# Kernel tuning notes

Measured on AMD Instinct MI355X. Metric: run time of the kernel, lower is better.

Reference implementation:

```python
import jax, jax.numpy as jnp
import numpy as np

N_NODES = 50000
N_EDGES = 800000
IN_FEATS = 1024
LAYERS = [128, 128]
EPS = 1e-5  # BatchNorm1d eps


def setup_inputs() -> dict:
    key = jax.random.key(0)
    ks = jax.random.split(key, 24)
    inp = {}
    inp["in_feat"] = jax.random.normal(ks[0], (N_NODES, IN_FEATS), jnp.float32)
    inp["src"] = jax.random.randint(ks[1], (N_EDGES,), 0, N_NODES, dtype=jnp.int32)
    inp["dst"] = jax.random.randint(ks[2], (N_EDGES,), 0, N_NODES, dtype=jnp.int32)
    dims = [IN_FEATS] + LAYERS
    i = 3
    for l in range(len(LAYERS)):
        din, dout = dims[l], dims[l + 1]
        s = 1.0 / np.sqrt(din)
        inp[f"W{l}"] = jax.random.uniform(ks[i], (din, dout), jnp.float32, -s, s); i += 1
        inp[f"b{l}"] = jnp.zeros((dout,), jnp.float32)
        inp[f"Wr{l}"] = jax.random.uniform(ks[i], (din, dout), jnp.float32, -s, s); i += 1
        inp[f"br{l}"] = jnp.zeros((dout,), jnp.float32)
        inp[f"gamma{l}"] = jnp.ones((dout,), jnp.float32)
        inp[f"beta{l}"] = jnp.zeros((dout,), jnp.float32)
        inp[f"mean{l}"] = jnp.zeros((dout,), jnp.float32)
        inp[f"var{l}"] = jnp.ones((dout,), jnp.float32)
    s = 1.0 / np.sqrt(LAYERS[-1])
    inp["Wd"] = jax.random.uniform(ks[i], (LAYERS[-1], 2), jnp.float32, -s, s)
    inp["bd"] = jnp.zeros((2,), jnp.float32)
    return inp


def gcn_layer(h, src, dst, W, b, Wr, br, gamma, beta, mean, var):
    # dgllife GCNLayer: GraphConv(norm='none', activation=relu) -> residual -> dropout(id, eval) -> BN(eval)
    msg = (h @ W)[src]                                        # [E, dout] gather of transformed src feats
    agg = jax.ops.segment_sum(msg, dst, num_segments=N_NODES)  # scatter-add to dst nodes
    new = jax.nn.relu(agg + b)                                 # GraphConv bias + activation
    res = jax.nn.relu(h @ Wr + br)                             # residual Linear + activation
    new = new + res
    return (new - mean) * jax.lax.rsqrt(var + EPS) * gamma + beta  # BatchNorm1d eval


def reference(in_feat, src, dst,
              W0, b0, Wr0, br0, gamma0, beta0, mean0, var0,
              W1, b1, Wr1, br1, gamma1, beta1, mean1, var1,
              Wd, bd):
    h = gcn_layer(in_feat, src, dst, W0, b0, Wr0, br0, gamma0, beta0, mean0, var0)
    h = gcn_layer(h, src, dst, W1, b1, Wr1, br1, gamma1, beta1, mean1, var1)
    logits = h @ Wd + bd                                       # [N, 2]
    return jax.nn.softmax(logits, axis=1)
```

## Files before the change

kernel.cpp:

```cpp
#include <hip/hip_runtime.h>
#include <math.h>

#define NNODES 50000
#define NEDGES 800000
#define KIN 1024
#define DH 128

typedef __bf16 bf16x8 __attribute__((ext_vector_type(8)));
typedef float floatx4 __attribute__((ext_vector_type(4)));

__global__ void k_zero2(int* __restrict__ a, int* __restrict__ b, int n) {
  int i = blockIdx.x * blockDim.x + threadIdx.x;
  if (i < n) { a[i] = 0; b[i] = 0; }
}

__global__ void k_hist(const int* __restrict__ dst, int* __restrict__ cnt, int E) {
  int i = blockIdx.x * blockDim.x + threadIdx.x;
  if (i < E) atomicAdd(&cnt[dst[i]], 1);
}

__global__ __launch_bounds__(1024) void k_scan_local(const int* __restrict__ cnt,
                                                     int* __restrict__ row_ptr,
                                                     int* __restrict__ bsum, int n) {
  __shared__ int sd[1024];
  int t = threadIdx.x;
  int i = blockIdx.x * 1024 + t;
  int v = (i < n) ? cnt[i] : 0;
  sd[t] = v;
  __syncthreads();
  for (int off = 1; off < 1024; off <<= 1) {
    int tv = (t >= off) ? sd[t - off] : 0;
    __syncthreads();
    sd[t] += tv;
    __syncthreads();
  }
  if (i < n) row_ptr[i] = sd[t] - v;
  if (t == 1023) bsum[blockIdx.x] = sd[t];
}

__global__ void k_scan_sums(const int* __restrict__ bsum, int* __restrict__ boff,
                            int nb, int* __restrict__ row_ptr, int n) {
  int lane = threadIdx.x;
  int v = (lane < nb) ? bsum[lane] : 0;
  int incl = v;
  for (int off = 1; off < 64; off <<= 1) {
    int t = __shfl_up(incl, off);
    if (lane >= off) incl += t;
  }
  boff[lane] = incl - v;
  if (lane == 63) row_ptr[n] = incl;
}

__global__ void k_scan_add(int* __restrict__ row_ptr, const int* __restrict__ boff, int n) {
  int i = blockIdx.x * blockDim.x + threadIdx.x;
  if (i < n) row_ptr[i] += boff[i >> 10];
}

__global__ void k_fill(const int* __restrict__ src, const int* __restrict__ dst,
                       const int* __restrict__ row_ptr, int* __restrict__ cursor,
                       int* __restrict__ csr_src, int E) {
  int i = blockIdx.x * blockDim.x + threadIdx.x;
  if (i < E) {
    int d = dst[i];
    int pos = row_ptr[d] + atomicAdd(&cursor[d], 1);
    csr_src[pos] = src[i];
  }
}

__global__ __launch_bounds__(256) void k_prepF(const float* __restrict__ W,
                                               const float* __restrict__ Wr,
                                               __bf16* __restrict__ Bf) {
  const int id = blockIdx.x * 256 + threadIdx.x;
  const int lane = id & 63;
  const int ks = (id >> 6) & 1;
  const int nt = (id >> 7) & 15;
  const int kb = id >> 11;
  const int n = nt * 16 + (lane & 15);
  const int k0 = kb * 64 + ks * 32 + (lane >> 4) * 8;
  bf16x8 h;
#pragma unroll
  for (int j = 0; j < 8; ++j) {
    const int k = k0 + j;
    const float v = (n < DH) ? W[(size_t)k * DH + n] : Wr[(size_t)k * DH + (n - DH)];
    h[j] = (__bf16)v;
  }
  *(bf16x8*)&Bf[(size_t)id * 8] = h;
}

template <typename AT, int K>
__global__ __launch_bounds__(256) void k_gemm3(
    const AT* __restrict__ X, const __bf16* __restrict__ Bf,
    const float* __restrict__ br, __bf16* __restrict__ XW,
    float* __restrict__ RES, int M) {
  constexpr unsigned ABYTES = 32u * K * 2u;
  constexpr unsigned SMEM = (ABYTES > 32768u) ? ABYTES : 32768u;
  __shared__ alignas(16) char smem[SMEM];
  __bf16* As = (__bf16*)smem;
  const int tid = threadIdx.x;
  const int lane = tid & 63;
  const int w = tid >> 6;
  const int l15 = lane & 15;
  const int quad = lane >> 4;
  const int bm0 = blockIdx.x * 32;

  {
    const int row = tid >> 3;
    int grow = bm0 + row;
    if (grow > M - 1) grow = M - 1;
    const AT* ap = X + (size_t)grow * K;
#pragma unroll 4
    for (int j = 0; j < K / 64; ++j) {
      const int c = (tid & 7) + 8 * j;
      bf16x8 h;
      if constexpr (sizeof(AT) == 4) {
        const float4 u = *(const float4*)(ap + c * 8);
        const float4 v = *(const float4*)(ap + c * 8 + 4);
        h[0] = (__bf16)u.x; h[1] = (__bf16)u.y; h[2] = (__bf16)u.z; h[3] = (__bf16)u.w;
        h[4] = (__bf16)v.x; h[5] = (__bf16)v.y; h[6] = (__bf16)v.z; h[7] = (__bf16)v.w;
      } else {
        h = *(const bf16x8*)(ap + c * 8);
      }
      const int cs = (c & ~7) | ((c ^ row) & 7);
      *(bf16x8*)&As[(size_t)row * K + (cs << 3)] = h;
    }
  }
  __syncthreads();

  floatx4 acc[2][4];
#pragma unroll
  for (int i = 0; i < 2; ++i)
#pragma unroll
    for (int j = 0; j < 4; ++j) acc[i][j] = (floatx4)0.f;

#pragma unroll 2
  for (int kb = 0; kb < K / 64; ++kb) {
    bf16x8 bfr[4][2];
#pragma unroll
    for (int nt = 0; nt < 4; ++nt)
#pragma unroll
      for (int ks = 0; ks < 2; ++ks) {
        const int ntg = (w << 2) + nt;
        const size_t idx = ((((size_t)kb * 16 + ntg) * 2 + ks) * 64 + lane) * 8;
        bfr[nt][ks] = *(const bf16x8*)(Bf + idx);
      }
    bf16x8 af[2][2];
#pragma unroll
    for (int mt = 0; mt < 2; ++mt)
#pragma unroll
      for (int ks = 0; ks < 2; ++ks) {
        const int row = mt * 16 + l15;
        const int c = kb * 8 + ks * 4 + quad;
        const int cs = (c & ~7) | ((c ^ row) & 7);
        af[mt][ks] = *(const bf16x8*)&As[(size_t)row * K + (cs << 3)];
      }
#pragma unroll
    for (int ks = 0; ks < 2; ++ks)
#pragma unroll
      for (int mt = 0; mt < 2; ++mt)
#pragma unroll
        for (int nt = 0; nt < 4; ++nt)
          acc[mt][nt] = __builtin_amdgcn_mfma_f32_16x16x32_bf16(af[mt][ks], bfr[nt][ks],
                                                                acc[mt][nt], 0, 0, 0);
  }

  __syncthreads();
  float* Cb = (float*)smem;
#pragma unroll
  for (int mt = 0; mt < 2; ++mt)
#pragma unroll
    for (int nt = 0; nt < 4; ++nt)
#pragma unroll
      for (int r = 0; r < 4; ++r)
        Cb[(mt * 16 + quad * 4 + r) * 256 + ((w << 6) + nt * 16 + l15)] = acc[mt][nt][r];
  __syncthreads();
  const int row = tid >> 3;
  const int seg = tid & 7;
  const int grow = bm0 + row;
  if (grow < M) {
    if (seg < 4) {
      const int c0 = seg * 32;
#pragma unroll
      for (int j = 0; j < 4; ++j) {
        const float4 v0 = *(const float4*)&Cb[row * 256 + c0 + j * 8];
        const float4 v1 = *(const float4*)&Cb[row * 256 + c0 + j * 8 + 4];
        bf16x8 h;
        h[0] = (__bf16)v0.x; h[1] = (__bf16)v0.y; h[2] = (__bf16)v0.z; h[3] = (__bf16)v0.w;
        h[4] = (__bf16)v1.x; h[5] = (__bf16)v1.y; h[6] = (__bf16)v1.z; h[7] = (__bf16)v1.w;
        *(bf16x8*)&XW[(size_t)grow * DH + c0 + j * 8] = h;
      }
    } else {
      const int c0 = (seg - 4) * 32;
#pragma unroll
      for (int j = 0; j < 8; ++j) {
        const float4 v = *(const float4*)&Cb[row * 256 + 128 + c0 + j * 4];
        const float4 bb = *(const float4*)&br[c0 + j * 4];
        *(float4*)&RES[(size_t)grow * DH + c0 + j * 4] =
            make_float4(fmaxf(v.x + bb.x, 0.f), fmaxf(v.y + bb.y, 0.f),
                        fmaxf(v.z + bb.z, 0.f), fmaxf(v.w + bb.w, 0.f));
      }
    }
  }
}

template <int MODE>
__global__ __launch_bounds__(256) void k_agg2(
    const __bf16* __restrict__ XW, const float* __restrict__ RES,
    const int* __restrict__ row_ptr, const int* __restrict__ csr_src,
    const float* __restrict__ b, const float* __restrict__ gamma,
    const float* __restrict__ beta, const float* __restrict__ mean,
    const float* __restrict__ var, const float* __restrict__ Wd,
    const float* __restrict__ bd, void* __restrict__ hout, int M) {
  const int node = (blockIdx.x << 2) + (threadIdx.x >> 6);
  const int lane = threadIdx.x & 63;
  if (node >= M) return;
  const int s = row_ptr[node], e = row_ptr[node + 1];
  const unsigned* xw = (const unsigned*)XW;
  float ax = 0.f, ay = 0.f;
  int i = s;
  for (; i + 3 < e; i += 4) {
    const int s0 = csr_src[i], s1 = csr_src[i + 1], s2 = csr_src[i + 2], s3 = csr_src[i + 3];
    const unsigned u0 = xw[(size_t)s0 * 64 + lane];
    const unsigned u1 = xw[(size_t)s1 * 64 + lane];
    const unsigned u2 = xw[(size_t)s2 * 64 + lane];
    const unsigned u3 = xw[(size_t)s3 * 64 + lane];
    ax += __uint_as_float(u0 << 16) + __uint_as_float(u1 << 16) +
          __uint_as_float(u2 << 16) + __uint_as_float(u3 << 16);
    ay += __uint_as_float(u0 & 0xffff0000u) + __uint_as_float(u1 & 0xffff0000u) +
          __uint_as_float(u2 & 0xffff0000u) + __uint_as_float(u3 & 0xffff0000u);
  }
  for (; i < e; ++i) {
    const unsigned u = xw[(size_t)csr_src[i] * 64 + lane];
    ax += __uint_as_float(u << 16);
    ay += __uint_as_float(u & 0xffff0000u);
  }
  const int f0 = lane << 1;
  const float2 bb = *(const float2*)&b[f0];
  const float2 rr = *(const float2*)&RES[(size_t)node * DH + f0];
  const float2 mm = *(const float2*)&mean[f0];
  const float2 vv = *(const float2*)&var[f0];
  const float2 gg = *(const float2*)&gamma[f0];
  const float2 be = *(const float2*)&beta[f0];
  const float x0 = fmaxf(ax + bb.x, 0.f) + rr.x;
  const float x1 = fmaxf(ay + bb.y, 0.f) + rr.y;
  const float y0 = (x0 - mm.x) * rsqrtf(vv.x + 1e-5f) * gg.x + be.x;
  const float y1 = (x1 - mm.y) * rsqrtf(vv.y + 1e-5f) * gg.y + be.y;
  if (MODE == 0) {
    union { __bf16 h[2]; unsigned u; } pk;
    pk.h[0] = (__bf16)y0;
    pk.h[1] = (__bf16)y1;
    ((unsigned*)hout)[(size_t)node * 64 + lane] = pk.u;
  } else {
    const float4 wv = *(const float4*)&Wd[f0 * 2];
    float l0 = y0 * wv.x + y1 * wv.z;
    float l1 = y0 * wv.y + y1 * wv.w;
#pragma unroll
    for (int off = 32; off > 0; off >>= 1) {
      l0 += __shfl_down(l0, off);
      l1 += __shfl_down(l1, off);
    }
    if (lane == 0) {
      l0 += bd[0];
      l1 += bd[1];
      const float m = fmaxf(l0, l1);
      const float e0 = expf(l0 - m), e1 = expf(l1 - m);
      const float inv = 1.f / (e0 + e1);
      float* out = (float*)hout;
      out[(size_t)node * 2] = e0 * inv;
      out[(size_t)node * 2 + 1] = e1 * inv;
    }
  }
}

extern "C" void kernel_launch(void* const* d_in, const int* in_sizes, int n_in,
                              void* d_out, int out_size, void* d_ws, size_t ws_size,
                              hipStream_t stream) {
  const float* in_feat = (const float*)d_in[0];
  const int* src = (const int*)d_in[1];
  const int* dst = (const int*)d_in[2];
  const float* W0 = (const float*)d_in[3];
  const float* b0 = (const float*)d_in[4];
  const float* Wr0 = (const float*)d_in[5];
  const float* br0 = (const float*)d_in[6];
  const float* gamma0 = (const float*)d_in[7];
  const float* beta0 = (const float*)d_in[8];
  const float* mean0 = (const float*)d_in[9];
  const float* var0 = (const float*)d_in[10];
  const float* W1 = (const float*)d_in[11];
  const float* b1 = (const float*)d_in[12];
  const float* Wr1 = (const float*)d_in[13];
  const float* br1 = (const float*)d_in[14];
  const float* gamma1 = (const float*)d_in[15];
  const float* beta1 = (const float*)d_in[16];
  const float* mean1 = (const float*)d_in[17];
  const float* var1 = (const float*)d_in[18];
  const float* Wd = (const float*)d_in[19];
  const float* bd = (const float*)d_in[20];
  float* out = (float*)d_out;

  char* ws = (char*)d_ws;
  size_t off = 0;
  auto alloc = [&](size_t bytes) {
    void* p = ws + off;
    off += (bytes + 255) & ~(size_t)255;
    return p;
  };
  __bf16* XWb = (__bf16*)alloc(sizeof(__bf16) * (size_t)NNODES * DH);
  __bf16* h1 = (__bf16*)alloc(sizeof(__bf16) * (size_t)NNODES * DH);
  float* RES = (float*)alloc(sizeof(float) * (size_t)NNODES * DH);
  int* cnt = (int*)alloc(sizeof(int) * NNODES);
  int* cursor = (int*)alloc(sizeof(int) * NNODES);
  int* row_ptr = (int*)alloc(sizeof(int) * (NNODES + 1));
  int* csr_src = (int*)alloc(sizeof(int) * NEDGES);
  int* bsum = (int*)alloc(sizeof(int) * 64);
  int* boff = (int*)alloc(sizeof(int) * 64);
  __bf16* Bf0 = (__bf16*)alloc(sizeof(__bf16) * 256 * KIN);
  __bf16* Bf1 = (__bf16*)alloc(sizeof(__bf16) * 256 * DH);

  const int nb = (NNODES + 1023) / 1024;
  k_zero2<<<(NNODES + 255) / 256, 256, 0, stream>>>(cnt, cursor, NNODES);
  k_hist<<<(NEDGES + 255) / 256, 256, 0, stream>>>(dst, cnt, NEDGES);
  k_scan_local<<<nb, 1024, 0, stream>>>(cnt, row_ptr, bsum, NNODES);
  k_scan_sums<<<1, 64, 0, stream>>>(bsum, boff, nb, row_ptr, NNODES);
  k_scan_add<<<(NNODES + 255) / 256, 256, 0, stream>>>(row_ptr, boff, NNODES);
  k_fill<<<(NEDGES + 255) / 256, 256, 0, stream>>>(src, dst, row_ptr, cursor, csr_src, NEDGES);

  k_prepF<<<(KIN / 64) * 16 * 2 * 64 / 256, 256, 0, stream>>>(W0, Wr0, Bf0);
  k_prepF<<<(DH / 64) * 16 * 2 * 64 / 256, 256, 0, stream>>>(W1, Wr1, Bf1);

  const int ggrid = (NNODES + 31) / 32;
  const int agrid = (NNODES + 3) / 4;
  k_gemm3<float, KIN><<<ggrid, 256, 0, stream>>>(in_feat, Bf0, br0, XWb, RES, NNODES);
  k_agg2<0><<<agrid, 256, 0, stream>>>(XWb, RES, row_ptr, csr_src, b0, gamma0, beta0,
                                       mean0, var0, nullptr, nullptr, h1, NNODES);
  k_gemm3<__bf16, DH><<<ggrid, 256, 0, stream>>>(h1, Bf1, br1, XWb, RES, NNODES);
  k_agg2<1><<<agrid, 256, 0, stream>>>(XWb, RES, row_ptr, csr_src, b1, gamma1, beta1,
                                       mean1, var1, Wd, bd, out, NNODES);
}
```

Baseline: 567.8 us.

## Load GEMM A fragments directly from global, interleave bf16 residual, shuffle-broadcast edge indices

Result: slower. 625.1 us (+10.1%).

```diff
diff --git a/kernel.cpp b/kernel.cpp
--- a/kernel.cpp
+++ b/kernel.cpp
@@ -88,14 +88,10 @@
 }
 
 template <typename AT, int K>
-__global__ __launch_bounds__(256) void k_gemm3(
+__global__ __launch_bounds__(256, 3) void k_gemm4(
     const AT* __restrict__ X, const __bf16* __restrict__ Bf,
-    const float* __restrict__ br, __bf16* __restrict__ XW,
-    float* __restrict__ RES, int M) {
-  constexpr unsigned ABYTES = 32u * K * 2u;
-  constexpr unsigned SMEM = (ABYTES > 32768u) ? ABYTES : 32768u;
-  __shared__ alignas(16) char smem[SMEM];
-  __bf16* As = (__bf16*)smem;
+    const float* __restrict__ br, __bf16* __restrict__ XR, int M) {
+  __shared__ alignas(16) float Cb[32 * 256];
   const int tid = threadIdx.x;
   const int lane = tid & 63;
   const int w = tid >> 6;
@@ -103,28 +99,10 @@
   const int quad = lane >> 4;
   const int bm0 = blockIdx.x * 32;
 
-  {
-    const int row = tid >> 3;
-    int grow = bm0 + row;
-    if (grow > M - 1) grow = M - 1;
-    const AT* ap = X + (size_t)grow * K;
-#pragma unroll 4
-    for (int j = 0; j < K / 64; ++j) {
-      const int c = (tid & 7) + 8 * j;
-      bf16x8 h;
-      if constexpr (sizeof(AT) == 4) {
-        const float4 u = *(const float4*)(ap + c * 8);
-        const float4 v = *(const float4*)(ap + c * 8 + 4);
-        h[0] = (__bf16)u.x; h[1] = (__bf16)u.y; h[2] = (__bf16)u.z; h[3] = (__bf16)u.w;
-        h[4] = (__bf16)v.x; h[5] = (__bf16)v.y; h[6] = (__bf16)v.z; h[7] = (__bf16)v.w;
-      } else {
-        h = *(const bf16x8*)(ap + c * 8);
-      }
-      const int cs = (c & ~7) | ((c ^ row) & 7);
-      *(bf16x8*)&As[(size_t)row * K + (cs << 3)] = h;
-    }
-  }
-  __syncthreads();
+  int r0 = bm0 + l15;      if (r0 > M - 1) r0 = M - 1;
+  int r1 = bm0 + 16 + l15; if (r1 > M - 1) r1 = M - 1;
+  const AT* a0 = X + (size_t)r0 * K + quad * 8;
+  const AT* a1 = X + (size_t)r1 * K + quad * 8;
 
   floatx4 acc[2][4];
 #pragma unroll
@@ -145,14 +123,25 @@
       }
     bf16x8 af[2][2];
 #pragma unroll
-    for (int mt = 0; mt < 2; ++mt)
-#pragma unroll
-      for (int ks = 0; ks < 2; ++ks) {
-        const int row = mt * 16 + l15;
-        const int c = kb * 8 + ks * 4 + quad;
-        const int cs = (c & ~7) | ((c ^ row) & 7);
-        af[mt][ks] = *(const bf16x8*)&As[(size_t)row * K + (cs << 3)];
-      }
+    for (int ks = 0; ks < 2; ++ks) {
+      const int ko = kb * 64 + ks * 32;
+      if constexpr (sizeof(AT) == 4) {
+        const float4 u0 = *(const float4*)(a0 + ko);
+        const float4 u1 = *(const float4*)(a0 + ko + 4);
+        const float4 v0 = *(const float4*)(a1 + ko);
+        const float4 v1 = *(const float4*)(a1 + ko + 4);
+        bf16x8 h0, h1;
+        h0[0] = (__bf16)u0.x; h0[1] = (__bf16)u0.y; h0[2] = (__bf16)u0.z; h0[3] = (__bf16)u0.w;
+        h0[4] = (__bf16)u1.x; h0[5] = (__bf16)u1.y; h0[6] = (__bf16)u1.z; h0[7] = (__bf16)u1.w;
+        h1[0] = (__bf16)v0.x; h1[1] = (__bf16)v0.y; h1[2] = (__bf16)v0.z; h1[3] = (__bf16)v0.w;
+        h1[4] = (__bf16)v1.x; h1[5] = (__bf16)v1.y; h1[6] = (__bf16)v1.z; h1[7] = (__bf16)v1.w;
+        af[0][ks] = h0;
+        af[1][ks] = h1;
+      } else {
+        af[0][ks] = *(const bf16x8*)(a0 + ko);
+        af[1][ks] = *(const bf16x8*)(a1 + ko);
+      }
+    }
 #pragma unroll
     for (int ks = 0; ks < 2; ++ks)
 #pragma unroll
@@ -163,8 +152,6 @@
                                                                 acc[mt][nt], 0, 0, 0);
   }
 
-  __syncthreads();
-  float* Cb = (float*)smem;
 #pragma unroll
   for (int mt = 0; mt < 2; ++mt)
 #pragma unroll
@@ -177,8 +164,8 @@
   const int seg = tid & 7;
   const int grow = bm0 + row;
   if (grow < M) {
+    const int c0 = (seg & 3) * 32;
     if (seg < 4) {
-      const int c0 = seg * 32;
 #pragma unroll
       for (int j = 0; j < 4; ++j) {
         const float4 v0 = *(const float4*)&Cb[row * 256 + c0 + j * 8];
@@ -186,62 +173,76 @@
         bf16x8 h;
         h[0] = (__bf16)v0.x; h[1] = (__bf16)v0.y; h[2] = (__bf16)v0.z; h[3] = (__bf16)v0.w;
         h[4] = (__bf16)v1.x; h[5] = (__bf16)v1.y; h[6] = (__bf16)v1.z; h[7] = (__bf16)v1.w;
-        *(bf16x8*)&XW[(size_t)grow * DH + c0 + j * 8] = h;
+        *(bf16x8*)&XR[(size_t)grow * 256 + c0 + j * 8] = h;
       }
     } else {
-      const int c0 = (seg - 4) * 32;
-#pragma unroll
-      for (int j = 0; j < 8; ++j) {
-        const float4 v = *(const float4*)&Cb[row * 256 + 128 + c0 + j * 4];
-        const float4 bb = *(const float4*)&br[c0 + j * 4];
-        *(float4*)&RES[(size_t)grow * DH + c0 + j * 4] =
-            make_float4(fmaxf(v.x + bb.x, 0.f), fmaxf(v.y + bb.y, 0.f),
-                        fmaxf(v.z + bb.z, 0.f), fmaxf(v.w + bb.w, 0.f));
+#pragma unroll
+      for (int j = 0; j < 4; ++j) {
+        const float4 v0 = *(const float4*)&Cb[row * 256 + 128 + c0 + j * 8];
+        const float4 v1 = *(const float4*)&Cb[row * 256 + 128 + c0 + j * 8 + 4];
+        const float4 b0 = *(const float4*)&br[c0 + j * 8];
+        const float4 b1 = *(const float4*)&br[c0 + j * 8 + 4];
+        bf16x8 h;
+        h[0] = (__bf16)fmaxf(v0.x + b0.x, 0.f); h[1] = (__bf16)fmaxf(v0.y + b0.y, 0.f);
+        h[2] = (__bf16)fmaxf(v0.z + b0.z, 0.f); h[3] = (__bf16)fmaxf(v0.w + b0.w, 0.f);
+        h[4] = (__bf16)fmaxf(v1.x + b1.x, 0.f); h[5] = (__bf16)fmaxf(v1.y + b1.y, 0.f);
+        h[6] = (__bf16)fmaxf(v1.z + b1.z, 0.f); h[7] = (__bf16)fmaxf(v1.w + b1.w, 0.f);
+        *(bf16x8*)&XR[(size_t)grow * 256 + 128 + c0 + j * 8] = h;
       }
     }
   }
 }
 
 template <int MODE>
-__global__ __launch_bounds__(256) void k_agg2(
-    const __bf16* __restrict__ XW, const float* __restrict__ RES,
-    const int* __restrict__ row_ptr, const int* __restrict__ csr_src,
-    const float* __restrict__ b, const float* __restrict__ gamma,
-    const float* __restrict__ beta, const float* __restrict__ mean,
-    const float* __restrict__ var, const float* __restrict__ Wd,
-    const float* __restrict__ bd, void* __restrict__ hout, int M) {
+__global__ __launch_bounds__(256) void k_agg3(
+    const __bf16* __restrict__ XR, const int* __restrict__ row_ptr,
+    const int* __restrict__ csr_src, const float* __restrict__ b,
+    const float* __restrict__ gamma, const float* __restrict__ beta,
+    const float* __restrict__ mean, const float* __restrict__ var,
+    const float* __restrict__ Wd, const float* __restrict__ bd,
+    void* __restrict__ hout, int M) {
   const int node = (blockIdx.x << 2) + (threadIdx.x >> 6);
   const int lane = threadIdx.x & 63;
   if (node >= M) return;
   const int s = row_ptr[node], e = row_ptr[node + 1];
-  const unsigned* xw = (const unsigned*)XW;
+  const unsigned* xr = (const unsigned*)XR;
   float ax = 0.f, ay = 0.f;
-  int i = s;
-  for (; i + 3 < e; i += 4) {
-    const int s0 = csr_src[i], s1 = csr_src[i + 1], s2 = csr_src[i + 2], s3 = csr_src[i + 3];
-    const unsigned u0 = xw[(size_t)s0 * 64 + lane];
-    const unsigned u1 = xw[(size_t)s1 * 64 + lane];
-    const unsigned u2 = xw[(size_t)s2 * 64 + lane];
-    const unsigned u3 = xw[(size_t)s3 * 64 + lane];
-    ax += __uint_as_float(u0 << 16) + __uint_as_float(u1 << 16) +
-          __uint_as_float(u2 << 16) + __uint_as_float(u3 << 16);
-    ay += __uint_as_float(u0 & 0xffff0000u) + __uint_as_float(u1 & 0xffff0000u) +
-          __uint_as_float(u2 & 0xffff0000u) + __uint_as_float(u3 & 0xffff0000u);
-  }
-  for (; i < e; ++i) {
-    const unsigned u = xw[(size_t)csr_src[i] * 64 + lane];
-    ax += __uint_as_float(u << 16);
-    ay += __uint_as_float(u & 0xffff0000u);
-  }
+  for (int base = s; base < e; base += 64) {
+    const int cnt = min(e - base, 64);
+    int li = base + lane; if (li > e - 1) li = e - 1;
+    const int myi = csr_src[li];
+    int j = 0;
+    for (; j + 8 <= cnt; j += 8) {
+      unsigned u[8];
+#pragma unroll
+      for (int t = 0; t < 8; ++t) {
+        const int sj = __shfl(myi, j + t);
+        u[t] = xr[(size_t)sj * 128 + lane];
+      }
+#pragma unroll
+      for (int t = 0; t < 8; ++t) {
+        ax += __uint_as_float(u[t] << 16);
+        ay += __uint_as_float(u[t] & 0xffff0000u);
+      }
+    }
+    for (; j < cnt; ++j) {
+      const int sj = __shfl(myi, j);
+      const unsigned u = xr[(size_t)sj * 128 + lane];
+      ax += __uint_as_float(u << 16);
+      ay += __uint_as_float(u & 0xffff0000u);
+    }
+  }
+  const unsigned ru = xr[(size_t)node * 128 + 64 + lane];
+  const float rx = __uint_as_float(ru << 16);
+  const float ry = __uint_as_float(ru & 0xffff0000u);
   const int f0 = lane << 1;
   const float2 bb = *(const float2*)&b[f0];
-  const float2 rr = *(const float2*)&RES[(size_t)node * DH + f0];
   const float2 mm = *(const float2*)&mean[f0];
   const float2 vv = *(const float2*)&var[f0];
   const float2 gg = *(const float2*)&gamma[f0];
   const float2 be = *(const float2*)&beta[f0];
-  const float x0 = fmaxf(ax + bb.x, 0.f) + rr.x;
-  const float x1 = fmaxf(ay + bb.y, 0.f) + rr.y;
+  const float x0 = fmaxf(ax + bb.x, 0.f) + rx;
+  const float x1 = fmaxf(ay + bb.y, 0.f) + ry;
   const float y0 = (x0 - mm.x) * rsqrtf(vv.x + 1e-5f) * gg.x + be.x;
   const float y1 = (x1 - mm.y) * rsqrtf(vv.y + 1e-5f) * gg.y + be.y;
   if (MODE == 0) {
@@ -304,9 +305,8 @@
     off += (bytes + 255) & ~(size_t)255;
     return p;
   };
-  __bf16* XWb = (__bf16*)alloc(sizeof(__bf16) * (size_t)NNODES * DH);
+  __bf16* XR = (__bf16*)alloc(sizeof(__bf16) * (size_t)NNODES * 256);
   __bf16* h1 = (__bf16*)alloc(sizeof(__bf16) * (size_t)NNODES * DH);
-  float* RES = (float*)alloc(sizeof(float) * (size_t)NNODES * DH);
   int* cnt = (int*)alloc(sizeof(int) * NNODES);
   int* cursor = (int*)alloc(sizeof(int) * NNODES);
   int* row_ptr = (int*)alloc(sizeof(int) * (NNODES + 1));
@@ -329,10 +329,10 @@
 
   const int ggrid = (NNODES + 31) / 32;
   const int agrid = (NNODES + 3) / 4;
-  k_gemm3<float, KIN><<<ggrid, 256, 0, stream>>>(in_feat, Bf0, br0, XWb, RES, NNODES);
-  k_agg2<0><<<agrid, 256, 0, stream>>>(XWb, RES, row_ptr, csr_src, b0, gamma0, beta0,
+  k_gemm4<float, KIN><<<ggrid, 256, 0, stream>>>(in_feat, Bf0, br0, XR, NNODES);
+  k_agg3<0><<<agrid, 256, 0, stream>>>(XR, row_ptr, csr_src, b0, gamma0, beta0,
                                        mean0, var0, nullptr, nullptr, h1, NNODES);
-  k_gemm3<__bf16, DH><<<ggrid, 256, 0, stream>>>(h1, Bf1, br1, XWb, RES, NNODES);
-  k_agg2<1><<<agrid, 256, 0, stream>>>(XWb, RES, row_ptr, csr_src, b1, gamma1, beta1,
+  k_gemm4<__bf16, DH><<<ggrid, 256, 0, stream>>>(h1, Bf1, br1, XR, NNODES);
+  k_agg3<1><<<agrid, 256, 0, stream>>>(XR, row_ptr, csr_src, b1, gamma1, beta1,
                                        mean1, var1, Wd, bd, out, NNODES);
 }
```
